# Kernel tuning notes

Measured on AMD Instinct MI355X. Metric: run time of the kernel, lower is better.

## Reference

```python
import jax, jax.numpy as jnp
import numpy as np

B, SQ, SK, D, H = 2, 2048, 2048, 1024, 16
DK = D // H


def setup_inputs() -> dict:
    key = jax.random.key(0)
    ks = jax.random.split(key, 9)
    query = jax.random.normal(ks[0], (B, SQ, D), dtype=jnp.float32)
    k_in = jax.random.normal(ks[1], (B, SK, D), dtype=jnp.float32)
    v_in = jax.random.normal(ks[2], (B, SK, D), dtype=jnp.float32)
    # padding mask: 1 for valid tokens, 0 for padding; lengths in [SK//2, SK]
    lengths = jax.random.randint(ks[3], (B,), SK // 2, SK + 1)
    mask = (jnp.arange(SK)[None, :] < lengths[:, None]).astype(jnp.int32)
    scale = 1.0 / np.sqrt(D)
    Wq = jax.random.normal(ks[4], (D, D), dtype=jnp.float32) * scale
    Wk = jax.random.normal(ks[5], (D, D), dtype=jnp.float32) * scale
    Wv = jax.random.normal(ks[6], (D, D), dtype=jnp.float32) * scale
    Wo = jax.random.normal(ks[7], (D, D), dtype=jnp.float32) * scale
    return {"query": query, "key": k_in, "value": v_in, "mask": mask,
            "Wq": Wq, "Wk": Wk, "Wv": Wv, "Wo": Wo}


def reference(query, key, value, mask, Wq, Wk, Wv, Wo):
    # linear projections (torch Linear: x @ W.T)
    q = (query @ Wq.T).reshape(B, SQ, H, DK).transpose(0, 2, 1, 3)  # [B,H,SQ,DK]
    k = (key @ Wk.T).reshape(B, SK, H, DK).transpose(0, 2, 1, 3)    # [B,H,SK,DK]
    v = (value @ Wv.T).reshape(B, SK, H, DK).transpose(0, 2, 1, 3)  # [B,H,SK,DK]
    scores = jnp.einsum('bhqd,bhkd->bhqk', q, k) / jnp.sqrt(jnp.float32(DK))
    # padding mask: (B, SK) -> (B, 1, 1, SK)
    scores = jnp.where(mask[:, None, None, :] == 0, -jnp.inf, scores)
    # future (causal) mask
    future = jnp.triu(jnp.ones((SQ, SK), dtype=bool), k=1)
    scores = jnp.where(future[None, None], -jnp.inf, scores)
    attn = jax.nn.softmax(scores, axis=-1)
    attn = jnp.nan_to_num(attn, nan=0.0)
    ctx = jnp.einsum('bhqk,bhkd->bhqd', attn, v)
    ctx = ctx.transpose(0, 2, 1, 3).reshape(B, SQ, D)
    return ctx @ Wo.T
```

## Files before the change

kernel.cpp:

```cpp
#include <hip/hip_runtime.h>
#include <hip/hip_bf16.h>
#include <stdint.h>

#define BB 2
#define SS 2048
#define DD 1024
#define HH 16
#define DKK 64
#define MM (BB*SS)
#define LOG2E 1.4426950408889634f
#define QSCALE (0.125f * LOG2E)

typedef __attribute__((ext_vector_type(8))) short short8;
typedef __attribute__((ext_vector_type(4))) float f32x4;

__device__ __forceinline__ short bfr(float f) {
    return (short)((__float_as_uint(f) + 0x8000u) >> 16);
}
__device__ __forceinline__ short8 cvt8(float4 a, float4 b) {
    short8 s;
    s[0] = bfr(a.x); s[1] = bfr(a.y); s[2] = bfr(a.z); s[3] = bfr(a.w);
    s[4] = bfr(b.x); s[5] = bfr(b.y); s[6] = bfr(b.z); s[7] = bfr(b.w);
    return s;
}

__device__ __forceinline__ void dma16(const void* g, void* l) {
    __builtin_amdgcn_global_load_lds(
        (const __attribute__((address_space(1))) uint32_t*)g,
        (__attribute__((address_space(3))) uint32_t*)(uintptr_t)l, 16, 0, 0);
}


__global__ __launch_bounds__(256) void cvt_all(const float* __restrict__ q,
                                               const float* __restrict__ k,
                                               const float* __restrict__ v,
                                               const float* __restrict__ wq,
                                               const float* __restrict__ wk,
                                               const float* __restrict__ wv,
                                               const float* __restrict__ wo,
                                               short* __restrict__ dst) {
    const size_t nth = (size_t)gridDim.x * blockDim.x;
    const size_t tid = (size_t)blockIdx.x * blockDim.x + threadIdx.x;
    for (size_t i8 = tid; i8 < (1u << 21); i8 += nth) {
        const size_t e = i8 * 8;
        const float* s;
        size_t rel;
        if (e < 4194304)        { s = q; rel = e; }
        else if (e < 8388608)   { s = k; rel = e - 4194304; }
        else if (e < 12582912)  { s = v; rel = e - 8388608; }
        else {
            const size_t we = e - 12582912;
            s = (we < 1048576) ? wq : (we < 2097152) ? wk : (we < 3145728) ? wv : wo;
            rel = we & 1048575;
        }
        const float4* p = (const float4*)(s + rel);
        *(short8*)(dst + e) = cvt8(p[0], p[1]);
    }
}

__global__ __launch_bounds__(256) void qkv_lds(const short* __restrict__ Abf,
                                               const short* __restrict__ Wbf,
                                               short* __restrict__ Qb,
                                               short* __restrict__ Kp,
                                               short* __restrict__ Vp) {
    __shared__ __align__(16) short As[128 * 32];
    __shared__ __align__(16) short Ws[128 * 32];
    const int z = blockIdx.z;
    const short* A = Abf + (size_t)z * 4194304;
    const short* W = Wbf + (size_t)z * 1048576;
    const int t = threadIdx.x, wave = t >> 6, lane = t & 63;
    const int la = lane & 15, quad = lane >> 4;
    const int wm = wave & 1, wn = wave >> 1;
    const int m0 = blockIdx.x * 128, n0 = blockIdx.y * 128;

    f32x4 acc[4][4];
    #pragma unroll
    for (int i = 0; i < 4; ++i)
        #pragma unroll
        for (int j = 0; j < 4; ++j) acc[i][j] = {0.f, 0.f, 0.f, 0.f};

    const int c0 = t, c1 = 256 + t;

    for (int k0 = 0; k0 < DD; k0 += 32) {
        dma16(A + (size_t)(m0 + (c0 >> 2)) * DD + k0 + (c0 & 3) * 8, (short*)As + c0 * 8);
        dma16(A + (size_t)(m0 + (c1 >> 2)) * DD + k0 + (c1 & 3) * 8, (short*)As + c1 * 8);
        dma16(W + (size_t)(n0 + (c0 >> 2)) * DD + k0 + (c0 & 3) * 8, (short*)Ws + c0 * 8);
        dma16(W + (size_t)(n0 + (c1 >> 2)) * DD + k0 + (c1 & 3) * 8, (short*)Ws + c1 * 8);
        __syncthreads();
        short8 af[4], bf[4];
        #pragma unroll
        for (int mt = 0; mt < 4; ++mt)
            af[mt] = *(const short8*)&As[(wm * 64 + mt * 16 + la) * 32 + quad * 8];
        #pragma unroll
        for (int nt = 0; nt < 4; ++nt)
            bf[nt] = *(const short8*)&Ws[(wn * 64 + nt * 16 + la) * 32 + quad * 8];
        #pragma unroll
        for (int mt = 0; mt < 4; ++mt)
            #pragma unroll
            for (int nt = 0; nt < 4; ++nt)
                acc[mt][nt] = __builtin_amdgcn_mfma_f32_16x16x32_bf16(af[mt], bf[nt], acc[mt][nt], 0, 0, 0);
        __syncthreads();
    }

    #pragma unroll
    for (int mt = 0; mt < 4; ++mt) {
        #pragma unroll
        for (int nt = 0; nt < 4; ++nt) {
            #pragma unroll
            for (int r = 0; r < 4; ++r) {
                const int m = m0 + wm * 64 + mt * 16 + quad * 4 + r;
                const int n = n0 + wn * 64 + nt * 16 + la;
                const int b = m >> 11, s = m & (SS - 1);
                const int h = n >> 6,  dk = n & 63;
                const int bh = b * HH + h;
                const float v = acc[mt][nt][r];
                if (z == 0) {
                    Qb[((size_t)bh * SS + s) * DKK + dk] = bfr(v * QSCALE);
                } else if (z == 1) {
                    Kp[((size_t)(bh * 32 + (s >> 6)) * 64 + (s & 63)) * 72 + dk] = bfr(v);
                } else {
                    Vp[((size_t)(bh * 32 + (s >> 6)) * 64 + dk) * 72 + (s & 63)] = bfr(v);
                }
            }
        }
    }
}

__global__ __launch_bounds__(128) void attn2(const short* __restrict__ Q,
                                             const short* __restrict__ Kp,
                                             const short* __restrict__ Vp,
                                             const int* __restrict__ mask,
                                             short* __restrict__ ctx) {
    const int b = blockIdx.z, h = blockIdx.y, x = blockIdx.x;
    const int t = threadIdx.x, wave = t >> 6, lane = t & 63;
    const int la = lane & 15, quad = lane >> 4;
    const int bh = b * HH + h;

    __shared__ __align__(16) short Ks[64 * 72];
    __shared__ __align__(16) short Vs[64 * 72];
    __shared__ __align__(16) short Ps[64 * 72];

    const short* Kt0 = Kp + (size_t)bh * 32 * 4608;
    const short* Vt0 = Vp + (size_t)bh * 32 * 4608;

    #pragma unroll 1
    for (int phase = 0; phase < 2; ++phase) {
        const int qt = phase ? x : (31 - x);
        short8 aq[2][2];
        #pragma unroll
        for (int mt = 0; mt < 2; ++mt)
            #pragma unroll
            for (int hf = 0; hf < 2; ++hf)
                aq[mt][hf] = *(const short8*)(Q + ((size_t)bh * SS + qt * 64 + wave * 32 + mt * 16 + la) * DKK
                                              + hf * 32 + quad * 8);

        float rs[2][4] = {};
        f32x4 o[2][4];
        #pragma unroll
        for (int mt = 0; mt < 2; ++mt)
            #pragma unroll
            for (int dc = 0; dc < 4; ++dc) o[mt][dc] = {0.f, 0.f, 0.f, 0.f};

        for (int kt = 0; kt <= qt; ++kt) {
            {
                const short* src = (wave == 0) ? (Kt0 + (size_t)kt * 4608) : (Vt0 + (size_t)kt * 4608);
                short* dst = (wave == 0) ? Ks : Vs;
                #pragma unroll
                for (int j = 0; j < 9; ++j)
                    dma16(src + j * 512 + lane * 8, dst + j * 512 + lane * 8);
            }
            __syncthreads();

            f32x4 s[2][4];
            #pragma unroll
            for (int mt = 0; mt < 2; ++mt)
                #pragma unroll
                for (int ct = 0; ct < 4; ++ct) s[mt][ct] = {0.f, 0.f, 0.f, 0.f};
            #pragma unroll
            for (int ct = 0; ct < 4; ++ct) {
                short8 kb0 = *(const short8*)&Ks[(ct * 16 + la) * 72 + quad * 8];
                short8 kb1 = *(const short8*)&Ks[(ct * 16 + la) * 72 + 32 + quad * 8];
                #pragma unroll
                for (int mt = 0; mt < 2; ++mt) {
                    s[mt][ct] = __builtin_amdgcn_mfma_f32_16x16x32_bf16(aq[mt][0], kb0, s[mt][ct], 0, 0, 0);
                    s[mt][ct] = __builtin_amdgcn_mfma_f32_16x16x32_bf16(aq[mt][1], kb1, s[mt][ct], 0, 0, 0);
                }
            }

            const bool diag   = (kt == qt);
            const bool padded = (kt >= 16);
            #pragma unroll
            for (int ct = 0; ct < 4; ++ct) {
                const int col = kt * 64 + ct * 16 + la;
                const int mv = padded ? mask[b * SS + col] : 1;
                #pragma unroll
                for (int mt = 0; mt < 2; ++mt) {
                    const int row0 = qt * 64 + wave * 32 + mt * 16 + quad * 4;
                    #pragma unroll
                    for (int r = 0; r < 4; ++r) {
                        const bool dead = (diag && col > row0 + r) || (padded && mv == 0);
                        const float p = dead ? 0.f : exp2f(s[mt][ct][r]);
                        rs[mt][r] += p;
                        Ps[(wave * 32 + mt * 16 + quad * 4 + r) * 72 + ct * 16 + la] = bfr(p);
                    }
                }
            }

            #pragma unroll
            for (int c2 = 0; c2 < 2; ++c2) {
                short8 pa[2];
                #pragma unroll
                for (int mt = 0; mt < 2; ++mt)
                    pa[mt] = *(const short8*)&Ps[(wave * 32 + mt * 16 + la) * 72 + c2 * 32 + quad * 8];
                #pragma unroll
                for (int dc = 0; dc < 4; ++dc) {
                    short8 vb = *(const short8*)&Vs[(dc * 16 + la) * 72 + c2 * 32 + quad * 8];
                    #pragma unroll
                    for (int mt = 0; mt < 2; ++mt)
                        o[mt][dc] = __builtin_amdgcn_mfma_f32_16x16x32_bf16(pa[mt], vb, o[mt][dc], 0, 0, 0);
                }
            }
            __syncthreads();
        }

        #pragma unroll
        for (int mt = 0; mt < 2; ++mt) {
            #pragma unroll
            for (int r = 0; r < 4; ++r) {
                float v = rs[mt][r];
                v += __shfl_xor(v, 1, 64);
                v += __shfl_xor(v, 2, 64);
                v += __shfl_xor(v, 4, 64);
                v += __shfl_xor(v, 8, 64);
                const float inv = 1.0f / v;
                const int qq = qt * 64 + wave * 32 + mt * 16 + quad * 4 + r;
                #pragma unroll
                for (int dc = 0; dc < 4; ++dc)
                    ctx[((size_t)(b * SS + qq) * DD) + h * DKK + dc * 16 + la] = bfr(o[mt][dc][r] * inv);
            }
        }
    }
}

__global__ __launch_bounds__(256) void o_lds(const short* __restrict__ Ctx,
                                             const short* __restrict__ Wob,
                                             float* __restrict__ out) {
    __shared__ __align__(16) short As[128 * 32];
    __shared__ __align__(16) short Ws[64 * 32];
    const int t = threadIdx.x, wave = t >> 6, lane = t & 63;
    const int la = lane & 15, quad = lane >> 4;
    const int wm = wave & 1, wn = wave >> 1;
    const int m0 = blockIdx.x * 128, n0 = blockIdx.y * 64;

    f32x4 acc[4][2];
    #pragma unroll
    for (int i = 0; i < 4; ++i)
        #pragma unroll
        for (int j = 0; j < 2; ++j) acc[i][j] = {0.f, 0.f, 0.f, 0.f};

    const int c0 = t, c1 = 256 + t;

    for (int k0 = 0; k0 < DD; k0 += 32) {
        dma16(Ctx + (size_t)(m0 + (c0 >> 2)) * DD + k0 + (c0 & 3) * 8, (short*)As + c0 * 8);
        dma16(Ctx + (size_t)(m0 + (c1 >> 2)) * DD + k0 + (c1 & 3) * 8, (short*)As + c1 * 8);
        dma16(Wob + (size_t)(n0 + (t >> 2)) * DD + k0 + (t & 3) * 8, (short*)Ws + t * 8);
        __syncthreads();
        short8 af[4], bf[2];
        #pragma unroll
        for (int mt = 0; mt < 4; ++mt)
            af[mt] = *(const short8*)&As[(wm * 64 + mt * 16 + la) * 32 + quad * 8];
        #pragma unroll
        for (int nt = 0; nt < 2; ++nt)
            bf[nt] = *(const short8*)&Ws[(wn * 32 + nt * 16 + la) * 32 + quad * 8];
        #pragma unroll
        for (int mt = 0; mt < 4; ++mt)
            #pragma unroll
            for (int nt = 0; nt < 2; ++nt)
                acc[mt][nt] = __builtin_amdgcn_mfma_f32_16x16x32_bf16(af[mt], bf[nt], acc[mt][nt], 0, 0, 0);
        __syncthreads();
    }

    #pragma unroll
    for (int mt = 0; mt < 4; ++mt)
        #pragma unroll
        for (int nt = 0; nt < 2; ++nt)
            #pragma unroll
            for (int r = 0; r < 4; ++r) {
                const int m = m0 + wm * 64 + mt * 16 + quad * 4 + r;
                const int n = n0 + wn * 32 + nt * 16 + la;
                out[(size_t)m * DD + n] = acc[mt][nt][r];
            }
}

__global__ __launch_bounds__(256) void qkv_gemm(const float* __restrict__ Aq,
                                                const float* __restrict__ Ak,
                                                const float* __restrict__ Av,
                                                const float* __restrict__ Wq,
                                                const float* __restrict__ Wk,
                                                const float* __restrict__ Wv,
                                                short* __restrict__ Qb,
                                                short* __restrict__ Kb,
                                                short* __restrict__ Vtb) {
    __shared__ __align__(16) short As[2][128][40];
    __shared__ __align__(16) short Ws[2][128][40];
    const int z = blockIdx.z;
    const float* A = (z == 0) ? Aq : (z == 1) ? Ak : Av;
    const float* W = (z == 0) ? Wq : (z == 1) ? Wk : Wv;
    short* Y = (z == 0) ? Qb : (z == 1) ? Kb : Vtb;
    const int t = threadIdx.x, wave = t >> 6, lane = t & 63;
    const int la = lane & 15, quad = lane >> 4;
    const int wm = wave & 1, wn = wave >> 1;
    const int m0 = blockIdx.x * 128, n0 = blockIdx.y * 128;
    const int srow = t >> 1, scol = (t & 1) * 16;
    f32x4 acc[4][4];
    #pragma unroll
    for (int i = 0; i < 4; ++i)
        #pragma unroll
        for (int j = 0; j < 4; ++j) acc[i][j] = {0.f, 0.f, 0.f, 0.f};
    float4 ar[4], wr[4];
    auto loadG = [&](int i) {
        const int k0 = i * 32;
        const float4* pa = (const float4*)(A + (size_t)(m0 + srow) * DD + k0 + scol);
        ar[0] = pa[0]; ar[1] = pa[1]; ar[2] = pa[2]; ar[3] = pa[3];
        const float4* pw = (const float4*)(W + (size_t)(n0 + srow) * DD + k0 + scol);
        wr[0] = pw[0]; wr[1] = pw[1]; wr[2] = pw[2]; wr[3] = pw[3];
    };
    auto storeL = [&](int buf) {
        *(short8*)&As[buf][srow][scol]     = cvt8(ar[0], ar[1]);
        *(short8*)&As[buf][srow][scol + 8] = cvt8(ar[2], ar[3]);
        *(short8*)&Ws[buf][srow][scol]     = cvt8(wr[0], wr[1]);
        *(short8*)&Ws[buf][srow][scol + 8] = cvt8(wr[2], wr[3]);
    };
    loadG(0); storeL(0); __syncthreads();
    const int NIT = DD / 32;
    for (int i = 0; i < NIT; ++i) {
        if (i + 1 < NIT) loadG(i + 1);
        const int buf = i & 1;
        short8 af[4], bfv[4];
        #pragma unroll
        for (int mt = 0; mt < 4; ++mt)
            af[mt] = *(const short8*)&As[buf][wm * 64 + mt * 16 + la][quad * 8];
        #pragma unroll
        for (int nt = 0; nt < 4; ++nt)
            bfv[nt] = *(const short8*)&Ws[buf][wn * 64 + nt * 16 + la][quad * 8];
        #pragma unroll
        for (int mt = 0; mt < 4; ++mt)
            #pragma unroll
            for (int nt = 0; nt < 4; ++nt)
                acc[mt][nt] = __builtin_amdgcn_mfma_f32_16x16x32_bf16(af[mt], bfv[nt], acc[mt][nt], 0, 0, 0);
        if (i + 1 < NIT) { storeL((i + 1) & 1); __syncthreads(); }
    }
    #pragma unroll
    for (int mt = 0; mt < 4; ++mt)
        #pragma unroll
        for (int nt = 0; nt < 4; ++nt)
            #pragma unroll
            for (int r = 0; r < 4; ++r) {
                const int m = m0 + wm * 64 + mt * 16 + quad * 4 + r;
                const int n = n0 + wn * 64 + nt * 16 + la;
                const int b = m >> 11, s = m & (SS - 1);
                const int h = n >> 6, dk = n & 63;
                float v = acc[mt][nt][r];
                if (z == 0)      Y[(((size_t)(b * HH + h) * SS + s) * DKK) + dk] = bfr(v * QSCALE);
                else if (z == 1) Y[(((size_t)(b * HH + h) * SS + s) * DKK) + dk] = bfr(v);
                else             Y[(((size_t)(b * HH + h) * DKK + dk) * SS) + s] = bfr(v);
            }
}

__global__ __launch_bounds__(256) void attn_fused(const short* __restrict__ Q,
                                                  const short* __restrict__ K,
                                                  const short* __restrict__ Vt,
                                                  const int* __restrict__ mask,
                                                  short* __restrict__ ctx) {
    const int b = blockIdx.z, h = blockIdx.y, x = blockIdx.x;
    const int t = threadIdx.x, wave = t >> 6, lane = t & 63;
    const int la = lane & 15, quad = lane >> 4;
    __shared__ __align__(16) short Ks[2][64][72];
    __shared__ __align__(16) short Vs[2][64][72];
    __shared__ __align__(16) short Ps[64][72];
    const size_t kbase = ((size_t)(b * HH + h) * SS) * DKK;
    const size_t vbase = ((size_t)(b * HH + h) * DKK) * SS;
    const int srow = t >> 2, scol = (t & 3) * 16;
    short8 kr[2], vr[2];
    auto loadG = [&](int kt) {
        const short* kp = K + kbase + (size_t)(kt * 64 + srow) * DKK + scol;
        kr[0] = ((const short8*)kp)[0]; kr[1] = ((const short8*)kp)[1];
        const short* vp = Vt + vbase + (size_t)srow * SS + kt * 64 + scol;
        vr[0] = ((const short8*)vp)[0]; vr[1] = ((const short8*)vp)[1];
    };
    auto storeL = [&](int buf) {
        *(short8*)&Ks[buf][srow][scol]     = kr[0];
        *(short8*)&Ks[buf][srow][scol + 8] = kr[1];
        *(short8*)&Vs[buf][srow][scol]     = vr[0];
        *(short8*)&Vs[buf][srow][scol + 8] = vr[1];
    };
    #pragma unroll 1
    for (int phase = 0; phase < 2; ++phase) {
        const int qt = phase ? x : (31 - x);
        const size_t qbase = kbase + (size_t)(qt * 64) * DKK;
        const short8 aq0 = *(const short8*)(Q + qbase + (size_t)(wave * 16 + la) * DKK + quad * 8);
        const short8 aq1 = *(const short8*)(Q + qbase + (size_t)(wave * 16 + la) * DKK + 32 + quad * 8);
        float rs[4] = {0.f, 0.f, 0.f, 0.f};
        f32x4 o[4];
        #pragma unroll
        for (int dc = 0; dc < 4; ++dc) o[dc] = {0.f, 0.f, 0.f, 0.f};
        const int nkt = qt + 1;
        loadG(0); storeL(0); __syncthreads();
        for (int kt = 0; kt < nkt; ++kt) {
            if (kt + 1 < nkt) loadG(kt + 1);
            const int buf = kt & 1;
            const bool diag = (kt == qt);
            const bool padded = (kt >= 16);
            f32x4 s[4];
            #pragma unroll
            for (int ct = 0; ct < 4; ++ct) {
                s[ct] = {0.f, 0.f, 0.f, 0.f};
                short8 kb0 = *(const short8*)&Ks[buf][ct * 16 + la][quad * 8];
                short8 kb1 = *(const short8*)&Ks[buf][ct * 16 + la][32 + quad * 8];
                s[ct] = __builtin_amdgcn_mfma_f32_16x16x32_bf16(aq0, kb0, s[ct], 0, 0, 0);
                s[ct] = __builtin_amdgcn_mfma_f32_16x16x32_bf16(aq1, kb1, s[ct], 0, 0, 0);
            }
            const int rowq = qt * 64 + wave * 16 + quad * 4;
            #pragma unroll
            for (int ct = 0; ct < 4; ++ct) {
                const int col = kt * 64 + ct * 16 + la;
                const int mv = padded ? mask[b * SS + col] : 1;
                #pragma unroll
                for (int r = 0; r < 4; ++r) {
                    const bool dead = (diag && col > rowq + r) || (padded && mv == 0);
                    const float p = dead ? 0.f : exp2f(s[ct][r]);
                    rs[r] += p;
                    Ps[wave * 16 + quad * 4 + r][ct * 16 + la] = bfr(p);
                }
            }
            #pragma unroll
            for (int c2 = 0; c2 < 2; ++c2) {
                short8 pa = *(const short8*)&Ps[wave * 16 + la][c2 * 32 + quad * 8];
                #pragma unroll
                for (int dc = 0; dc < 4; ++dc) {
                    short8 vb = *(const short8*)&Vs[buf][dc * 16 + la][c2 * 32 + quad * 8];
                    o[dc] = __builtin_amdgcn_mfma_f32_16x16x32_bf16(pa, vb, o[dc], 0, 0, 0);
                }
            }
            if (kt + 1 < nkt) { storeL((kt + 1) & 1); __syncthreads(); }
        }
        #pragma unroll
        for (int r = 0; r < 4; ++r) {
            float v = rs[r];
            v += __shfl_xor(v, 1, 64);
            v += __shfl_xor(v, 2, 64);
            v += __shfl_xor(v, 4, 64);
            v += __shfl_xor(v, 8, 64);
            const float inv = 1.0f / v;
            const int q = qt * 64 + wave * 16 + quad * 4 + r;
            #pragma unroll
            for (int dc = 0; dc < 4; ++dc)
                ctx[((size_t)(b * SS + q) * DD) + h * DKK + dc * 16 + la] = bfr(o[dc][r] * inv);
        }
        __syncthreads();
    }
}

__global__ __launch_bounds__(256) void o_gemm(const short* __restrict__ Ctx,
                                              const float* __restrict__ Wo,
                                              float* __restrict__ out) {
    __shared__ __align__(16) short As[2][128][40];
    __shared__ __align__(16) short Ws[2][64][40];
    const int t = threadIdx.x, wave = t >> 6, lane = t & 63;
    const int la = lane & 15, quad = lane >> 4;
    const int wm = wave & 1, wn = wave >> 1;
    const int m0 = blockIdx.x * 128, n0 = blockIdx.y * 64;
    const int srowA = t >> 1, scolA = (t & 1) * 16;
    const int srowW = t >> 2, scolW = (t & 3) * 8;
    f32x4 acc[4][2];
    #pragma unroll
    for (int i = 0; i < 4; ++i)
        #pragma unroll
        for (int j = 0; j < 2; ++j) acc[i][j] = {0.f, 0.f, 0.f, 0.f};
    short8 ab[2];
    float4 wr[2];
    auto loadG = [&](int i) {
        const int k0 = i * 32;
        const short8* pa = (const short8*)(Ctx + (size_t)(m0 + srowA) * DD + k0 + scolA);
        ab[0] = pa[0]; ab[1] = pa[1];
        const float4* pw = (const float4*)(Wo + (size_t)(n0 + srowW) * DD + k0 + scolW);
        wr[0] = pw[0]; wr[1] = pw[1];
    };
    auto storeL = [&](int buf) {
        *(short8*)&As[buf][srowA][scolA]     = ab[0];
        *(short8*)&As[buf][srowA][scolA + 8] = ab[1];
        *(short8*)&Ws[buf][srowW][scolW]     = cvt8(wr[0], wr[1]);
    };
    loadG(0); storeL(0); __syncthreads();
    const int NIT = DD / 32;
    for (int i = 0; i < NIT; ++i) {
        if (i + 1 < NIT) loadG(i + 1);
        const int buf = i & 1;
        short8 af[4], bfv[2];
        #pragma unroll
        for (int mt = 0; mt < 4; ++mt)
            af[mt] = *(const short8*)&As[buf][wm * 64 + mt * 16 + la][quad * 8];
        #pragma unroll
        for (int nt = 0; nt < 2; ++nt)
            bfv[nt] = *(const short8*)&Ws[buf][wn * 32 + nt * 16 + la][quad * 8];
        #pragma unroll
        for (int mt = 0; mt < 4; ++mt)
            #pragma unroll
            for (int nt = 0; nt < 2; ++nt)
                acc[mt][nt] = __builtin_amdgcn_mfma_f32_16x16x32_bf16(af[mt], bfv[nt], acc[mt][nt], 0, 0, 0);
        if (i + 1 < NIT) { storeL((i + 1) & 1); __syncthreads(); }
    }
    #pragma unroll
    for (int mt = 0; mt < 4; ++mt)
        #pragma unroll
        for (int nt = 0; nt < 2; ++nt)
            #pragma unroll
            for (int r = 0; r < 4; ++r) {
                const int m = m0 + wm * 64 + mt * 16 + quad * 4 + r;
                const int n = n0 + wn * 32 + nt * 16 + la;
                out[(size_t)m * DD + n] = acc[mt][nt][r];
            }
}

extern "C" void kernel_launch(void* const* d_in, const int* in_sizes, int n_in,
                              void* d_out, int out_size, void* d_ws, size_t ws_size,
                              hipStream_t stream) {
    (void)in_sizes; (void)n_in; (void)out_size;
    const float* query = (const float*)d_in[0];
    const float* key   = (const float*)d_in[1];
    const float* value = (const float*)d_in[2];
    const int*   mask  = (const int*)  d_in[3];
    const float* Wq    = (const float*)d_in[4];
    const float* Wk    = (const float*)d_in[5];
    const float* Wv    = (const float*)d_in[6];
    const float* Wo    = (const float*)d_in[7];
    dim3 tb(256);

    if (ws_size >= (size_t)61000000) {
        short* Abf = (short*)d_ws;
        short* Wbf = Abf + 12582912;
        short* Qb  = Abf + 16777216;
        short* Kp  = Abf + 20971520;
        short* Vp  = Abf + 25690112;
        short* Ctx = Abf;

        hipLaunchKernelGGL(cvt_all, dim3(1024), tb, 0, stream,
                           query, key, value, Wq, Wk, Wv, Wo, Abf);
        hipLaunchKernelGGL(qkv_lds, dim3(32, 8, 3), tb, 0, stream, Abf, Wbf, Qb, Kp, Vp);
        hipLaunchKernelGGL(attn2, dim3(16, 16, 2), dim3(128), 0, stream,
                           (const short*)Qb, (const short*)Kp, (const short*)Vp, mask, Ctx);
        hipLaunchKernelGGL(o_lds, dim3(32, 16), tb, 0, stream,
                           (const short*)Ctx, (const short*)(Wbf + 3145728), (float*)d_out);
    } else {
        short* Qb  = (short*)d_ws;
        short* Kb  = Qb + (size_t)BB * HH * SS * DKK;
        short* Vtb = Kb + (size_t)BB * HH * SS * DKK;
        short* Ctx = Vtb + (size_t)BB * HH * SS * DKK;
        hipLaunchKernelGGL(qkv_gemm, dim3(MM / 128, DD / 128, 3), tb, 0, stream,
                           query, key, value, Wq, Wk, Wv, Qb, Kb, Vtb);
        hipLaunchKernelGGL(attn_fused, dim3(SS / 128, HH, BB), tb, 0, stream,
                           (const short*)Qb, (const short*)Kb, (const short*)Vtb, mask, Ctx);
        hipLaunchKernelGGL(o_gemm, dim3(MM / 128, DD / 64), tb, 0, stream,
                           (const short*)Ctx, Wo, (float*)d_out);
    }
}
```

Before: 255.9 us.

## Rework GEMMs with XOR-swizzled 64-wide K tiles and register-prefetched attention kernel

The QKV and output GEMMs now stage 64-wide K slices into LDS using an XOR swizzle. This is meant to cut bank conflicts and halve the number of barriers per K step. The attention kernel is replaced by attn3, which uses one 64-row query tile per 256-thread block instead of a paired-phase 128-thread block, and prefetches the next K/V tile into registers while computing. The mask becomes an additive float bias precomputed in the conversion kernel, and K/V switch to plain row-major and transposed layouts. The causal work imbalance is no longer balanced within a block, and the LDS stores of the prefetched tile add two barriers per step.

```diff
diff --git a/kernel.cpp b/kernel.cpp
--- a/kernel.cpp
+++ b/kernel.cpp
@@ -38,9 +38,12 @@
                                                const float* __restrict__ wk,
                                                const float* __restrict__ wv,
                                                const float* __restrict__ wo,
-                                               short* __restrict__ dst) {
+                                               const int* __restrict__ mask,
+                                               short* __restrict__ dst,
+                                               float* __restrict__ Fb) {
     const size_t nth = (size_t)gridDim.x * blockDim.x;
     const size_t tid = (size_t)blockIdx.x * blockDim.x + threadIdx.x;
+    if (tid < BB * SS) Fb[tid] = mask[tid] ? 0.f : -30000.f;
     for (size_t i8 = tid; i8 < (1u << 21); i8 += nth) {
         const size_t e = i8 * 8;
         const float* s;
@@ -61,10 +64,10 @@
 __global__ __launch_bounds__(256) void qkv_lds(const short* __restrict__ Abf,
                                                const short* __restrict__ Wbf,
                                                short* __restrict__ Qb,
-                                               short* __restrict__ Kp,
-                                               short* __restrict__ Vp) {
-    __shared__ __align__(16) short As[128 * 32];
-    __shared__ __align__(16) short Ws[128 * 32];
+                                               short* __restrict__ Kb,
+                                               short* __restrict__ Vtb) {
+    __shared__ __align__(16) short As[128 * 64];
+    __shared__ __align__(16) short Ws[128 * 64];
     const int z = blockIdx.z;
     const short* A = Abf + (size_t)z * 4194304;
     const short* W = Wbf + (size_t)z * 1048576;
@@ -79,174 +82,165 @@
         #pragma unroll
         for (int j = 0; j < 4; ++j) acc[i][j] = {0.f, 0.f, 0.f, 0.f};
 
-    const int c0 = t, c1 = 256 + t;
-
-    for (int k0 = 0; k0 < DD; k0 += 32) {
-        dma16(A + (size_t)(m0 + (c0 >> 2)) * DD + k0 + (c0 & 3) * 8, (short*)As + c0 * 8);
-        dma16(A + (size_t)(m0 + (c1 >> 2)) * DD + k0 + (c1 & 3) * 8, (short*)As + c1 * 8);
-        dma16(W + (size_t)(n0 + (c0 >> 2)) * DD + k0 + (c0 & 3) * 8, (short*)Ws + c0 * 8);
-        dma16(W + (size_t)(n0 + (c1 >> 2)) * DD + k0 + (c1 & 3) * 8, (short*)Ws + c1 * 8);
+    for (int k0 = 0; k0 < DD; k0 += 64) {
+        #pragma unroll
+        for (int j = 0; j < 4; ++j) {
+            const int idx = j * 256 + t;
+            const int row = idx >> 3, cpos = idx & 7;
+            const int gc = cpos ^ (row & 7);
+            dma16(A + (size_t)(m0 + row) * DD + k0 + gc * 8, (short*)As + idx * 8);
+            dma16(W + (size_t)(n0 + row) * DD + k0 + gc * 8, (short*)Ws + idx * 8);
+        }
         __syncthreads();
-        short8 af[4], bf[4];
-        #pragma unroll
-        for (int mt = 0; mt < 4; ++mt)
-            af[mt] = *(const short8*)&As[(wm * 64 + mt * 16 + la) * 32 + quad * 8];
+        #pragma unroll
+        for (int kh = 0; kh < 2; ++kh) {
+            short8 af[4], bf[4];
+            #pragma unroll
+            for (int mt = 0; mt < 4; ++mt) {
+                const int row = wm * 64 + mt * 16 + la;
+                af[mt] = *(const short8*)&As[row * 64 + (((kh << 2) | quad) ^ (row & 7)) * 8];
+            }
+            #pragma unroll
+            for (int nt = 0; nt < 4; ++nt) {
+                const int row = wn * 64 + nt * 16 + la;
+                bf[nt] = *(const short8*)&Ws[row * 64 + (((kh << 2) | quad) ^ (row & 7)) * 8];
+            }
+            #pragma unroll
+            for (int mt = 0; mt < 4; ++mt)
+                #pragma unroll
+                for (int nt = 0; nt < 4; ++nt)
+                    acc[mt][nt] = __builtin_amdgcn_mfma_f32_16x16x32_bf16(af[mt], bf[nt], acc[mt][nt], 0, 0, 0);
+        }
+        __syncthreads();
+    }
+
+    #pragma unroll
+    for (int mt = 0; mt < 4; ++mt)
         #pragma unroll
         for (int nt = 0; nt < 4; ++nt)
-            bf[nt] = *(const short8*)&Ws[(wn * 64 + nt * 16 + la) * 32 + quad * 8];
-        #pragma unroll
-        for (int mt = 0; mt < 4; ++mt)
-            #pragma unroll
-            for (int nt = 0; nt < 4; ++nt)
-                acc[mt][nt] = __builtin_amdgcn_mfma_f32_16x16x32_bf16(af[mt], bf[nt], acc[mt][nt], 0, 0, 0);
-        __syncthreads();
-    }
-
-    #pragma unroll
-    for (int mt = 0; mt < 4; ++mt) {
-        #pragma unroll
-        for (int nt = 0; nt < 4; ++nt) {
             #pragma unroll
             for (int r = 0; r < 4; ++r) {
                 const int m = m0 + wm * 64 + mt * 16 + quad * 4 + r;
                 const int n = n0 + wn * 64 + nt * 16 + la;
                 const int b = m >> 11, s = m & (SS - 1);
-                const int h = n >> 6,  dk = n & 63;
+                const int h = n >> 6, dk = n & 63;
                 const int bh = b * HH + h;
                 const float v = acc[mt][nt][r];
-                if (z == 0) {
-                    Qb[((size_t)bh * SS + s) * DKK + dk] = bfr(v * QSCALE);
-                } else if (z == 1) {
-                    Kp[((size_t)(bh * 32 + (s >> 6)) * 64 + (s & 63)) * 72 + dk] = bfr(v);
-                } else {
-                    Vp[((size_t)(bh * 32 + (s >> 6)) * 64 + dk) * 72 + (s & 63)] = bfr(v);
-                }
-            }
-        }
-    }
-}
-
-__global__ __launch_bounds__(128) void attn2(const short* __restrict__ Q,
-                                             const short* __restrict__ Kp,
-                                             const short* __restrict__ Vp,
-                                             const int* __restrict__ mask,
+                if (z == 0)      Qb[((size_t)bh * SS + s) * DKK + dk] = bfr(v * QSCALE);
+                else if (z == 1) Kb[((size_t)bh * SS + s) * DKK + dk] = bfr(v);
+                else             Vtb[((size_t)bh * DKK + dk) * SS + s] = bfr(v);
+            }
+}
+
+__global__ __launch_bounds__(256) void attn3(const short* __restrict__ Q,
+                                             const short* __restrict__ K,
+                                             const short* __restrict__ Vt,
+                                             const float* __restrict__ Fb,
                                              short* __restrict__ ctx) {
-    const int b = blockIdx.z, h = blockIdx.y, x = blockIdx.x;
+    const int b = blockIdx.z, h = blockIdx.y;
+    const int qt = 31 - blockIdx.x;
     const int t = threadIdx.x, wave = t >> 6, lane = t & 63;
     const int la = lane & 15, quad = lane >> 4;
-    const int bh = b * HH + h;
-
-    __shared__ __align__(16) short Ks[64 * 72];
-    __shared__ __align__(16) short Vs[64 * 72];
-    __shared__ __align__(16) short Ps[64 * 72];
-
-    const short* Kt0 = Kp + (size_t)bh * 32 * 4608;
-    const short* Vt0 = Vp + (size_t)bh * 32 * 4608;
-
-    #pragma unroll 1
-    for (int phase = 0; phase < 2; ++phase) {
-        const int qt = phase ? x : (31 - x);
-        short8 aq[2][2];
-        #pragma unroll
-        for (int mt = 0; mt < 2; ++mt)
-            #pragma unroll
-            for (int hf = 0; hf < 2; ++hf)
-                aq[mt][hf] = *(const short8*)(Q + ((size_t)bh * SS + qt * 64 + wave * 32 + mt * 16 + la) * DKK
-                                              + hf * 32 + quad * 8);
-
-        float rs[2][4] = {};
-        f32x4 o[2][4];
-        #pragma unroll
-        for (int mt = 0; mt < 2; ++mt)
-            #pragma unroll
-            for (int dc = 0; dc < 4; ++dc) o[mt][dc] = {0.f, 0.f, 0.f, 0.f};
-
-        for (int kt = 0; kt <= qt; ++kt) {
-            {
-                const short* src = (wave == 0) ? (Kt0 + (size_t)kt * 4608) : (Vt0 + (size_t)kt * 4608);
-                short* dst = (wave == 0) ? Ks : Vs;
-                #pragma unroll
-                for (int j = 0; j < 9; ++j)
-                    dma16(src + j * 512 + lane * 8, dst + j * 512 + lane * 8);
-            }
+
+    __shared__ __align__(16) short Ks[64][72];
+    __shared__ __align__(16) short Vs[64][72];
+    __shared__ __align__(16) short Ps[64][72];
+
+    const size_t kbase = ((size_t)(b * HH + h) * SS) * DKK;
+    const size_t vbase = ((size_t)(b * HH + h) * DKK) * SS;
+
+    const short8 aq0 = *(const short8*)(Q + kbase + (size_t)(qt * 64 + wave * 16 + la) * DKK + quad * 8);
+    const short8 aq1 = *(const short8*)(Q + kbase + (size_t)(qt * 64 + wave * 16 + la) * DKK + 32 + quad * 8);
+
+    const int srow = t >> 2, scol = (t & 3) * 16;
+    short8 kr[2], vr[2];
+    auto loadG = [&](int kt) {
+        const short* kp = K + kbase + (size_t)(kt * 64 + srow) * DKK + scol;
+        kr[0] = ((const short8*)kp)[0]; kr[1] = ((const short8*)kp)[1];
+        const short* vp = Vt + vbase + (size_t)srow * SS + kt * 64 + scol;
+        vr[0] = ((const short8*)vp)[0]; vr[1] = ((const short8*)vp)[1];
+    };
+    auto storeL = [&]() {
+        *(short8*)&Ks[srow][scol]     = kr[0];
+        *(short8*)&Ks[srow][scol + 8] = kr[1];
+        *(short8*)&Vs[srow][scol]     = vr[0];
+        *(short8*)&Vs[srow][scol + 8] = vr[1];
+    };
+
+    float rs[4] = {0.f, 0.f, 0.f, 0.f};
+    f32x4 o[4];
+    #pragma unroll
+    for (int dc = 0; dc < 4; ++dc) o[dc] = {0.f, 0.f, 0.f, 0.f};
+
+    loadG(0); storeL(); __syncthreads();
+
+    for (int kt = 0; kt <= qt; ++kt) {
+        if (kt < qt) loadG(kt + 1);
+        const bool diag   = (kt == qt);
+        const bool padded = (kt >= 16);
+
+        f32x4 s[4];
+        #pragma unroll
+        for (int ct = 0; ct < 4; ++ct) {
+            s[ct] = {0.f, 0.f, 0.f, 0.f};
+            short8 kb0 = *(const short8*)&Ks[ct * 16 + la][quad * 8];
+            short8 kb1 = *(const short8*)&Ks[ct * 16 + la][32 + quad * 8];
+            s[ct] = __builtin_amdgcn_mfma_f32_16x16x32_bf16(aq0, kb0, s[ct], 0, 0, 0);
+            s[ct] = __builtin_amdgcn_mfma_f32_16x16x32_bf16(aq1, kb1, s[ct], 0, 0, 0);
+        }
+
+        const int rowq = qt * 64 + wave * 16 + quad * 4;
+        #pragma unroll
+        for (int ct = 0; ct < 4; ++ct) {
+            const int col = kt * 64 + ct * 16 + la;
+            const float bias = padded ? Fb[b * SS + col] : 0.f;
+            #pragma unroll
+            for (int r = 0; r < 4; ++r) {
+                float sv = s[ct][r] + bias;
+                if (diag && col > rowq + r) sv = -30000.f;
+                const float p = exp2f(sv);
+                rs[r] += p;
+                Ps[wave * 16 + quad * 4 + r][ct * 16 + la] = bfr(p);
+            }
+        }
+
+        #pragma unroll
+        for (int c2 = 0; c2 < 2; ++c2) {
+            short8 pa = *(const short8*)&Ps[wave * 16 + la][c2 * 32 + quad * 8];
+            #pragma unroll
+            for (int dc = 0; dc < 4; ++dc) {
+                short8 vb = *(const short8*)&Vs[dc * 16 + la][c2 * 32 + quad * 8];
+                o[dc] = __builtin_amdgcn_mfma_f32_16x16x32_bf16(pa, vb, o[dc], 0, 0, 0);
+            }
+        }
+
+        if (kt < qt) {
             __syncthreads();
-
-            f32x4 s[2][4];
-            #pragma unroll
-            for (int mt = 0; mt < 2; ++mt)
-                #pragma unroll
-                for (int ct = 0; ct < 4; ++ct) s[mt][ct] = {0.f, 0.f, 0.f, 0.f};
-            #pragma unroll
-            for (int ct = 0; ct < 4; ++ct) {
-                short8 kb0 = *(const short8*)&Ks[(ct * 16 + la) * 72 + quad * 8];
-                short8 kb1 = *(const short8*)&Ks[(ct * 16 + la) * 72 + 32 + quad * 8];
-                #pragma unroll
-                for (int mt = 0; mt < 2; ++mt) {
-                    s[mt][ct] = __builtin_amdgcn_mfma_f32_16x16x32_bf16(aq[mt][0], kb0, s[mt][ct], 0, 0, 0);
-                    s[mt][ct] = __builtin_amdgcn_mfma_f32_16x16x32_bf16(aq[mt][1], kb1, s[mt][ct], 0, 0, 0);
-                }
-            }
-
-            const bool diag   = (kt == qt);
-            const bool padded = (kt >= 16);
-            #pragma unroll
-            for (int ct = 0; ct < 4; ++ct) {
-                const int col = kt * 64 + ct * 16 + la;
-                const int mv = padded ? mask[b * SS + col] : 1;
-                #pragma unroll
-                for (int mt = 0; mt < 2; ++mt) {
-                    const int row0 = qt * 64 + wave * 32 + mt * 16 + quad * 4;
-                    #pragma unroll
-                    for (int r = 0; r < 4; ++r) {
-                        const bool dead = (diag && col > row0 + r) || (padded && mv == 0);
-                        const float p = dead ? 0.f : exp2f(s[mt][ct][r]);
-                        rs[mt][r] += p;
-                        Ps[(wave * 32 + mt * 16 + quad * 4 + r) * 72 + ct * 16 + la] = bfr(p);
-                    }
-                }
-            }
-
-            #pragma unroll
-            for (int c2 = 0; c2 < 2; ++c2) {
-                short8 pa[2];
-                #pragma unroll
-                for (int mt = 0; mt < 2; ++mt)
-                    pa[mt] = *(const short8*)&Ps[(wave * 32 + mt * 16 + la) * 72 + c2 * 32 + quad * 8];
-                #pragma unroll
-                for (int dc = 0; dc < 4; ++dc) {
-                    short8 vb = *(const short8*)&Vs[(dc * 16 + la) * 72 + c2 * 32 + quad * 8];
-                    #pragma unroll
-                    for (int mt = 0; mt < 2; ++mt)
-                        o[mt][dc] = __builtin_amdgcn_mfma_f32_16x16x32_bf16(pa[mt], vb, o[mt][dc], 0, 0, 0);
-                }
-            }
+            storeL();
             __syncthreads();
         }
-
-        #pragma unroll
-        for (int mt = 0; mt < 2; ++mt) {
-            #pragma unroll
-            for (int r = 0; r < 4; ++r) {
-                float v = rs[mt][r];
-                v += __shfl_xor(v, 1, 64);
-                v += __shfl_xor(v, 2, 64);
-                v += __shfl_xor(v, 4, 64);
-                v += __shfl_xor(v, 8, 64);
-                const float inv = 1.0f / v;
-                const int qq = qt * 64 + wave * 32 + mt * 16 + quad * 4 + r;
-                #pragma unroll
-                for (int dc = 0; dc < 4; ++dc)
-                    ctx[((size_t)(b * SS + qq) * DD) + h * DKK + dc * 16 + la] = bfr(o[mt][dc][r] * inv);
-            }
-        }
+    }
+
+    #pragma unroll
+    for (int r = 0; r < 4; ++r) {
+        float v = rs[r];
+        v += __shfl_xor(v, 1, 64);
+        v += __shfl_xor(v, 2, 64);
+        v += __shfl_xor(v, 4, 64);
+        v += __shfl_xor(v, 8, 64);
+        const float inv = 1.0f / v;
+        const int q = qt * 64 + wave * 16 + quad * 4 + r;
+        #pragma unroll
+        for (int dc = 0; dc < 4; ++dc)
+            ctx[((size_t)(b * SS + q) * DD) + h * DKK + dc * 16 + la] = bfr(o[dc][r] * inv);
     }
 }
 
 __global__ __launch_bounds__(256) void o_lds(const short* __restrict__ Ctx,
                                              const short* __restrict__ Wob,
                                              float* __restrict__ out) {
-    __shared__ __align__(16) short As[128 * 32];
-    __shared__ __align__(16) short Ws[64 * 32];
+    __shared__ __align__(16) short As[128 * 64];
+    __shared__ __align__(16) short Ws[64 * 64];
     const int t = threadIdx.x, wave = t >> 6, lane = t & 63;
     const int la = lane & 15, quad = lane >> 4;
     const int wm = wave & 1, wn = wave >> 1;
@@ -258,25 +252,41 @@
         #pragma unroll
         for (int j = 0; j < 2; ++j) acc[i][j] = {0.f, 0.f, 0.f, 0.f};
 
-    const int c0 = t, c1 = 256 + t;
-
-    for (int k0 = 0; k0 < DD; k0 += 32) {
-        dma16(Ctx + (size_t)(m0 + (c0 >> 2)) * DD + k0 + (c0 & 3) * 8, (short*)As + c0 * 8);
-        dma16(Ctx + (size_t)(m0 + (c1 >> 2)) * DD + k0 + (c1 & 3) * 8, (short*)As + c1 * 8);
-        dma16(Wob + (size_t)(n0 + (t >> 2)) * DD + k0 + (t & 3) * 8, (short*)Ws + t * 8);
+    for (int k0 = 0; k0 < DD; k0 += 64) {
+        #pragma unroll
+        for (int j = 0; j < 4; ++j) {
+            const int idx = j * 256 + t;
+            const int row = idx >> 3, cpos = idx & 7;
+            const int gc = cpos ^ (row & 7);
+            dma16(Ctx + (size_t)(m0 + row) * DD + k0 + gc * 8, (short*)As + idx * 8);
+        }
+        #pragma unroll
+        for (int j = 0; j < 2; ++j) {
+            const int idx = j * 256 + t;
+            const int row = idx >> 3, cpos = idx & 7;
+            const int gc = cpos ^ (row & 7);
+            dma16(Wob + (size_t)(n0 + row) * DD + k0 + gc * 8, (short*)Ws + idx * 8);
+        }
         __syncthreads();
-        short8 af[4], bf[2];
-        #pragma unroll
-        for (int mt = 0; mt < 4; ++mt)
-            af[mt] = *(const short8*)&As[(wm * 64 + mt * 16 + la) * 32 + quad * 8];
-        #pragma unroll
-        for (int nt = 0; nt < 2; ++nt)
-            bf[nt] = *(const short8*)&Ws[(wn * 32 + nt * 16 + la) * 32 + quad * 8];
-        #pragma unroll
-        for (int mt = 0; mt < 4; ++mt)
-            #pragma unroll
-            for (int nt = 0; nt < 2; ++nt)
-                acc[mt][nt] = __builtin_amdgcn_mfma_f32_16x16x32_bf16(af[mt], bf[nt], acc[mt][nt], 0, 0, 0);
+        #pragma unroll
+        for (int kh = 0; kh < 2; ++kh) {
+            short8 af[4], bf[2];
+            #pragma unroll
+            for (int mt = 0; mt < 4; ++mt) {
+                const int row = wm * 64 + mt * 16 + la;
+                af[mt] = *(const short8*)&As[row * 64 + (((kh << 2) | quad) ^ (row & 7)) * 8];
+            }
+            #pragma unroll
+            for (int nt = 0; nt < 2; ++nt) {
+                const int row = wn * 32 + nt * 16 + la;
+                bf[nt] = *(const short8*)&Ws[row * 64 + (((kh << 2) | quad) ^ (row & 7)) * 8];
+            }
+            #pragma unroll
+            for (int mt = 0; mt < 4; ++mt)
+                #pragma unroll
+                for (int nt = 0; nt < 2; ++nt)
+                    acc[mt][nt] = __builtin_amdgcn_mfma_f32_16x16x32_bf16(af[mt], bf[nt], acc[mt][nt], 0, 0, 0);
+        }
         __syncthreads();
     }
 
@@ -540,15 +550,16 @@
         short* Abf = (short*)d_ws;
         short* Wbf = Abf + 12582912;
         short* Qb  = Abf + 16777216;
-        short* Kp  = Abf + 20971520;
-        short* Vp  = Abf + 25690112;
+        short* Kb  = Abf + 20971520;
+        short* Vtb = Abf + 25165824;
+        float* Fb  = (float*)(Abf + 29360128);
         short* Ctx = Abf;
 
         hipLaunchKernelGGL(cvt_all, dim3(1024), tb, 0, stream,
-                           query, key, value, Wq, Wk, Wv, Wo, Abf);
-        hipLaunchKernelGGL(qkv_lds, dim3(32, 8, 3), tb, 0, stream, Abf, Wbf, Qb, Kp, Vp);
-        hipLaunchKernelGGL(attn2, dim3(16, 16, 2), dim3(128), 0, stream,
-                           (const short*)Qb, (const short*)Kp, (const short*)Vp, mask, Ctx);
+                           query, key, value, Wq, Wk, Wv, Wo, mask, Abf, Fb);
+        hipLaunchKernelGGL(qkv_lds, dim3(32, 8, 3), tb, 0, stream, Abf, Wbf, Qb, Kb, Vtb);
+        hipLaunchKernelGGL(attn3, dim3(32, 16, 2), tb, 0, stream,
+                           (const short*)Qb, (const short*)Kb, (const short*)Vtb, Fb, Ctx);
         hipLaunchKernelGGL(o_lds, dim3(32, 16), tb, 0, stream,
                            (const short*)Ctx, (const short*)(Wbf + 3145728), (float*)d_out);
     } else {
```

Result: slower. 264.8 us (+3.5%).
